# Optimization experiments

Hardware: AMD Instinct MI355X
Metric: run time of the kernel (lower is better)

Reference implementation:

```python
import jax, jax.numpy as jnp
import numpy as np

B, M = 4, 4096          # events x points-per-event (row_splits are uniform)
N = B * M
IN_DIM, SPACE, PROP, K = 128, 4, 64, 32


def setup_inputs() -> dict:
    key = jax.random.key(0)
    k1, k2, k3, k4, k5 = jax.random.split(key, 5)
    x = jax.random.normal(k1, (N, IN_DIM), jnp.float32)
    row_splits = (jnp.arange(B + 1, dtype=jnp.int32) * M)
    s = 1.0 / np.sqrt(IN_DIM)
    Ws = jax.random.uniform(k2, (IN_DIM, SPACE), jnp.float32, -s, s)
    bs = jax.random.uniform(k3, (SPACE,), jnp.float32, -s, s)
    Wp = jax.random.uniform(k4, (IN_DIM, PROP), jnp.float32, -s, s)
    bp = jax.random.uniform(k5, (PROP,), jnp.float32, -s, s)
    return {"x": x, "Ws": Ws, "bs": bs, "Wp": Wp, "bp": bp, "row_splits": row_splits}


def _gravnet(x, Ws, bs, Wp, bp):
    space = x @ Ws + bs                      # [N, SPACE] learned coordinates
    prop = x @ Wp + bp                       # [N, PROP]  features to propagate
    sp = space.reshape(B, M, SPACE)
    pr = prop.reshape(B, M, PROP)
    # exact KNN within each event (row_splits segment): pairwise squared dists
    sq = jnp.sum(sp * sp, axis=-1)                         # [B, M]
    d2 = sq[:, :, None] + sq[:, None, :] - 2.0 * jnp.einsum("bms,bns->bmn", sp, sp)
    neg_vals, idx = jax.lax.top_k(-d2, K)                  # k smallest dists (incl. self)
    distsq = jnp.maximum(-neg_vals, 0.0)                   # [B, M, K]
    weights = jnp.exp(-10.0 * distsq)                      # [B, M, K]
    gathered = jax.vmap(lambda p, i: p[i])(pr, idx)        # [B, M, K, PROP]
    weighted = gathered * weights[..., None]
    fmean = jnp.mean(weighted, axis=2)                     # [B, M, PROP]
    fmax = jnp.max(weighted, axis=2)                       # [B, M, PROP]
    out = jnp.concatenate([fmean, fmax], axis=-1)          # [B, M, 2*PROP]
    return out.reshape(N, 2 * PROP)


def reference(x, Ws, bs, Wp, bp, row_splits):
    # row_splits encodes uniform segments [0, M, 2M, ...]; KNN never crosses them.
    return _gravnet(x, Ws, bs, Wp, bp)
```

## Files before the change

### kernel.cpp

```cpp
#include <hip/hip_runtime.h>
#include <hip/hip_bf16.h>
#include <math.h>

#define N_TOT   16384
#define M_EV    4096
#define IN_DIM  128
#define SPACE_D 4
#define PROP_D  64
#define K_NN    32
#define CAND_CAP 128
#define MARGIN  0.04f

typedef _Float16 h2 __attribute__((ext_vector_type(2)));
typedef unsigned long long u64;

__device__ __forceinline__ h2 pkmin(h2 a, h2 b) {
#if __has_builtin(__builtin_elementwise_min)
  return __builtin_elementwise_min(a, b);
#else
  h2 r; r.x = (a.x < b.x) ? a.x : b.x; r.y = (a.y < b.y) ? a.y : b.y; return r;
#endif
}

__device__ __forceinline__ h2 pkrtz(float a, float b) {
  return __builtin_bit_cast(h2, __builtin_amdgcn_cvt_pkrtz(a, b));
}

__global__ __launch_bounds__(256) void linear_kernel(
    const float* __restrict__ x,
    const float* __restrict__ Ws, const float* __restrict__ bs,
    const float* __restrict__ Wp, const float* __restrict__ bp,
    float* __restrict__ space, float* __restrict__ prop)
{
  const int lane = threadIdx.x & 63;
  const int wid  = threadIdx.x >> 6;
  const int r0   = __builtin_amdgcn_readfirstlane((int)blockIdx.x * 16 + wid * 4);

  const float* xr = x + (size_t)r0 * IN_DIM;

  float a0 = bp[lane];
  float a1 = a0, a2 = a0, a3 = a0;
  #pragma unroll
  for (int i = 0; i < IN_DIM; ++i) {
    const float w = Wp[i * PROP_D + lane];
    a0 = fmaf(xr[i],              w, a0);
    a1 = fmaf(xr[IN_DIM + i],     w, a1);
    a2 = fmaf(xr[2 * IN_DIM + i], w, a2);
    a3 = fmaf(xr[3 * IN_DIM + i], w, a3);
  }
  prop[(size_t)(r0 + 0) * PROP_D + lane] = a0;
  prop[(size_t)(r0 + 1) * PROP_D + lane] = a1;
  prop[(size_t)(r0 + 2) * PROP_D + lane] = a2;
  prop[(size_t)(r0 + 3) * PROP_D + lane] = a3;

  if (lane < 16) {
    const int r = lane >> 2, c = lane & 3;
    const float* xq = x + (size_t)(r0 + r) * IN_DIM;
    float a = bs[c];
    #pragma unroll
    for (int i = 0; i < IN_DIM; ++i)
      a = fmaf(xq[i], Ws[i * SPACE_D + c], a);
    space[(size_t)(r0 + r) * SPACE_D + c] = a;
  }
}

__device__ __forceinline__ int mbcnt64(u64 mk) {
  return (int)__builtin_amdgcn_mbcnt_hi((unsigned)(mk >> 32),
           __builtin_amdgcn_mbcnt_lo((unsigned)mk, 0u));
}

__global__ __launch_bounds__(512, 8) void knn_kernel(
    const float4* __restrict__ space,
    const float*  __restrict__ prop,
    float*        __restrict__ out)
{
  const int lane = threadIdx.x & 63;
  const int wid  = threadIdx.x >> 6;
  const int row  = (int)blockIdx.x * 8 + wid;
  const int m0   = row & ~(M_EV - 1);
  const int mloc = row & (M_EV - 1);

  __shared__ uint4 s_pk[M_EV / 2];
  __shared__ int   s_ci[8][CAND_CAP];
  __shared__ uint2 s_w[8][K_NN];
  __shared__ int   s_cnt[8];

  {
    const float4* src = space + m0;
    #pragma unroll
    for (int it = 0; it < 4; ++it) {
      const int i = (int)threadIdx.x + it * 512;
      const float4 a = src[i];
      const float4 b = src[i + 2048];
      s_pk[i] = make_uint4(
        __builtin_bit_cast(unsigned, pkrtz(a.x, b.x)),
        __builtin_bit_cast(unsigned, pkrtz(a.y, b.y)),
        __builtin_bit_cast(unsigned, pkrtz(a.z, b.z)),
        __builtin_bit_cast(unsigned, pkrtz(a.w, b.w)));
    }
  }
  if (lane == 0) s_cnt[wid] = 0;
  __syncthreads();

  const float4 qf = space[m0 + mloc];
  const h2 qx = pkrtz(qf.x, qf.x), qy = pkrtz(qf.y, qf.y);
  const h2 qz = pkrtz(qf.z, qf.z), qw = pkrtz(qf.w, qf.w);

  unsigned pd[32];
  h2 mn; mn.x = (_Float16)65504.f; mn.y = (_Float16)65504.f;
  #pragma unroll
  for (int t = 0; t < 32; ++t) {
    const uint4 u = s_pk[lane + (t << 6)];
    const h2 dx = qx - __builtin_bit_cast(h2, u.x);
    const h2 dy = qy - __builtin_bit_cast(h2, u.y);
    const h2 dz = qz - __builtin_bit_cast(h2, u.z);
    const h2 dw = qw - __builtin_bit_cast(h2, u.w);
    h2 s = dx * dx;
    s = dy * dy + s;
    s = dz * dz + s;
    s = dw * dw + s;
    pd[t] = __builtin_bit_cast(unsigned, s);
    mn = pkmin(mn, s);
  }

  const unsigned mnbits = __builtin_bit_cast(unsigned, mn);
  const unsigned c0 = mnbits & 0xFFFFu, c1 = mnbits >> 16;
  unsigned blo = 0u, bhi = 0x7C00u;
  while (blo < bhi) {
    const unsigned mid = (blo + bhi) >> 1;
    const int c = (int)__popcll(__ballot(c0 <= mid)) +
                  (int)__popcll(__ballot(c1 <= mid));
    if (c >= K_NN) { bhi = mid; if (c == K_NN) break; }
    else blo = mid + 1;
  }
  const float T = (float)__builtin_bit_cast(_Float16, (unsigned short)bhi) + MARGIN;
  const h2 Th = pkrtz(T, T);

  #pragma unroll
  for (int t = 0; t < 32; ++t) asm volatile("" : "+v"(pd[t]));

  #pragma unroll
  for (int t = 0; t < 32; ++t) {
    const h2 s = __builtin_bit_cast(h2, pd[t]);
    if (s.x <= Th.x) {
      const int pos = atomicAdd(&s_cnt[wid], 1);
      if (pos < CAND_CAP) s_ci[wid][pos] = (t << 6) + lane;
    }
    if (s.y <= Th.y) {
      const int pos = atomicAdd(&s_cnt[wid], 1);
      if (pos < CAND_CAP) s_ci[wid][pos] = (t << 6) + lane + 2048;
    }
  }
  int C = s_cnt[wid];

  if (C > CAND_CAP) {
    const float4* __restrict__ ev = space + m0;
    unsigned lo = 0u, hi = __float_as_uint(T);
    while (lo < hi) {
      const unsigned mid = (lo + hi) >> 1;
      const float fm = __uint_as_float(mid);
      int c = 0;
      #pragma unroll 1
      for (int t = 0; t < 64; ++t) {
        const float4 cc = ev[lane + (t << 6)];
        const float dx = qf.x - cc.x, dy = qf.y - cc.y;
        const float dz = qf.z - cc.z, dw = qf.w - cc.w;
        const float dd = fmaf(dx, dx, fmaf(dy, dy, fmaf(dz, dz, dw * dw)));
        c += (int)__popcll(__ballot(dd <= fm));
      }
      if (c >= K_NN) { hi = mid; if (c == K_NN) break; }
      else lo = mid + 1;
    }
    const float Tf = __uint_as_float(hi);
    int cnt = 0;
    #pragma unroll 1
    for (int pass = 0; pass < 2; ++pass) {
      #pragma unroll 1
      for (int t = 0; t < 64; ++t) {
        const float4 cc = ev[lane + (t << 6)];
        const float dx = qf.x - cc.x, dy = qf.y - cc.y;
        const float dz = qf.z - cc.z, dw = qf.w - cc.w;
        const float dd = fmaf(dx, dx, fmaf(dy, dy, fmaf(dz, dz, dw * dw)));
        const bool p = pass ? (dd == Tf) : (dd < Tf);
        const u64 mk = __ballot(p);
        if (p) {
          const int pos = cnt + mbcnt64(mk);
          if (pos < K_NN) s_ci[wid][pos] = (t << 6) + lane;
        }
        cnt += (int)__popcll(mk);
      }
      if (cnt >= K_NN) break;
    }
    C = K_NN;
  }

  const bool h0 = (lane < C), h1 = (64 + lane < C);
  const int i0 = h0 ? s_ci[wid][lane]      : 0;
  const int i1 = h1 ? s_ci[wid][64 + lane] : 0;
  float v0 = INFINITY, v1 = INFINITY;
  if (h0) {
    const float4 cc = space[m0 + i0];
    const float dx = qf.x - cc.x, dy = qf.y - cc.y;
    const float dz = qf.z - cc.z, dw = qf.w - cc.w;
    v0 = fmaf(dx, dx, fmaf(dy, dy, fmaf(dz, dz, dw * dw)));
  }
  if (h1) {
    const float4 cc = space[m0 + i1];
    const float dx = qf.x - cc.x, dy = qf.y - cc.y;
    const float dz = qf.z - cc.z, dw = qf.w - cc.w;
    v1 = fmaf(dx, dx, fmaf(dy, dy, fmaf(dz, dz, dw * dw)));
  }

  unsigned lo = 0u, hi = __float_as_uint(T);
  while (lo < hi) {
    const unsigned mid = (lo + hi) >> 1;
    const float fm = __uint_as_float(mid);
    const int c = (int)__popcll(__ballot(v0 <= fm)) +
                  (int)__popcll(__ballot(v1 <= fm));
    if (c >= K_NN) { hi = mid; if (c == K_NN) break; }
    else lo = mid + 1;
  }
  const float T2 = __uint_as_float(hi);

  const u64 mkE0 = __ballot(v0 == T2);
  const u64 mkE1 = __ballot(v1 == T2);
  const int L = (int)__popcll(__ballot(v0 < T2)) +
                (int)__popcll(__ballot(v1 < T2));
  const int e = K_NN - L;
  const int nE0 = (int)__popcll(mkE0);
  const bool sel0 = (v0 < T2) || ((v0 == T2) && (mbcnt64(mkE0) < e));
  const bool sel1 = (v1 < T2) || ((v1 == T2) && (nE0 + mbcnt64(mkE1) < e));

  const float w0 = __expf(-10.f * v0);
  const float w1 = __expf(-10.f * v1);

  {
    const u64 mkS0 = __ballot(sel0);
    if (sel0) {
      const int pos = mbcnt64(mkS0);
      s_w[wid][pos] = make_uint2((unsigned)i0, __float_as_uint(w0));
    }
    const int b0 = (int)__popcll(mkS0);
    const u64 mkS1 = __ballot(sel1);
    if (sel1) {
      const int pos = b0 + mbcnt64(mkS1);
      s_w[wid][pos] = make_uint2((unsigned)i1, __float_as_uint(w1));
    }
  }

  float accm = 0.f;
  float accx = -INFINITY;
  const float* __restrict__ pb = prop + ((size_t)m0 << 6) + lane;
  #pragma unroll 8
  for (int n = 0; n < K_NN; ++n) {
    const uint2 wn = s_w[wid][n];
    const float w = __uint_as_float(wn.y);
    const float v = pb[(size_t)wn.x << 6];
    const float wv = w * v;
    accm += wv;
    accx = fmaxf(accx, wv);
  }
  out[(size_t)row * 128 + lane]      = accm * (1.f / K_NN);
  out[(size_t)row * 128 + 64 + lane] = accx;
}

extern "C" void kernel_launch(void* const* d_in, const int* in_sizes, int n_in,
                              void* d_out, int out_size, void* d_ws, size_t ws_size,
                              hipStream_t stream) {
  const float* x  = (const float*)d_in[0];
  const float* Ws = (const float*)d_in[1];
  const float* bs = (const float*)d_in[2];
  const float* Wp = (const float*)d_in[3];
  const float* bp = (const float*)d_in[4];
  float* out = (float*)d_out;

  float* prop  = (float*)d_ws;
  float* space = (float*)((char*)d_ws + (size_t)N_TOT * PROP_D * sizeof(float));

  linear_kernel<<<N_TOT / 16, 256, 0, stream>>>(x, Ws, bs, Wp, bp, space, prop);
  knn_kernel<<<N_TOT / 8, 512, 0, stream>>>((const float4*)space, prop, out);
}
```

Measured before the change: 52.99 us.

## Compute KNN distance prefilter with MFMA and process 32 query rows per block

Replaces the per-query packed-fp16 distance scan with MFMA 16x16x32 fp16 matrix products computing -2q·c plus a precomputed |c|^2 term. Each block now handles 32 queries: per-lane partial minima are reduced into a threshold per row, and a second MFMA pass collects candidates with atomic appends. The exact fp32 refinement, selection and gather stages are kept, run per row by each wave. The aim is to cut the VALU cost of the all-pairs scan and amortize the shared-memory staging of the event over more queries, at the cost of doing the MFMA pass twice, lower occupancy, and a fp16 expanded-form approximation that relies on a larger margin.

```diff
diff --git a/kernel.cpp b/kernel.cpp
--- a/kernel.cpp
+++ b/kernel.cpp
@@ -9,21 +9,27 @@
 #define PROP_D  64
 #define K_NN    32
 #define CAND_CAP 128
-#define MARGIN  0.04f
+#define M_SCALED 0.25f
 
 typedef _Float16 h2 __attribute__((ext_vector_type(2)));
+typedef __attribute__((ext_vector_type(8))) _Float16 h16x8;
+typedef __attribute__((ext_vector_type(4))) float f32x4;
 typedef unsigned long long u64;
-
-__device__ __forceinline__ h2 pkmin(h2 a, h2 b) {
-#if __has_builtin(__builtin_elementwise_min)
-  return __builtin_elementwise_min(a, b);
-#else
-  h2 r; r.x = (a.x < b.x) ? a.x : b.x; r.y = (a.y < b.y) ? a.y : b.y; return r;
-#endif
-}
 
 __device__ __forceinline__ h2 pkrtz(float a, float b) {
   return __builtin_bit_cast(h2, __builtin_amdgcn_cvt_pkrtz(a, b));
+}
+__device__ __forceinline__ unsigned fmap(float f) {
+  unsigned b = __float_as_uint(f);
+  return (b & 0x80000000u) ? ~b : (b | 0x80000000u);
+}
+__device__ __forceinline__ float funmap(unsigned u) {
+  unsigned b = (u & 0x80000000u) ? (u & 0x7FFFFFFFu) : ~u;
+  return __uint_as_float(b);
+}
+__device__ __forceinline__ int mbcnt64(u64 mk) {
+  return (int)__builtin_amdgcn_mbcnt_hi((unsigned)(mk >> 32),
+           __builtin_amdgcn_mbcnt_lo((unsigned)mk, 0u));
 }
 
 __global__ __launch_bounds__(256) void linear_kernel(
@@ -64,204 +70,242 @@
   }
 }
 
-__device__ __forceinline__ int mbcnt64(u64 mk) {
-  return (int)__builtin_amdgcn_mbcnt_hi((unsigned)(mk >> 32),
-           __builtin_amdgcn_mbcnt_lo((unsigned)mk, 0u));
-}
-
-__global__ __launch_bounds__(512, 8) void knn_kernel(
+__global__ __launch_bounds__(512, 4) void knn_kernel(
     const float4* __restrict__ space,
     const float*  __restrict__ prop,
     float*        __restrict__ out)
 {
   const int lane = threadIdx.x & 63;
   const int wid  = threadIdx.x >> 6;
-  const int row  = (int)blockIdx.x * 8 + wid;
-  const int m0   = row & ~(M_EV - 1);
-  const int mloc = row & (M_EV - 1);
-
-  __shared__ uint4 s_pk[M_EV / 2];
-  __shared__ int   s_ci[8][CAND_CAP];
-  __shared__ uint2 s_w[8][K_NN];
-  __shared__ int   s_cnt[8];
+  const int rt   = wid >> 2;
+  const int qq   = wid & 3;
+  const int brow0 = (int)blockIdx.x * 32;
+  const int m0    = brow0 & ~(M_EV - 1);
+  const int ml0   = brow0 & (M_EV - 1);
+
+  __shared__ uint2          s_B[M_EV];
+  __shared__ float          s_c2[M_EV];
+  __shared__ float          s_pmin[32][64];
+  __shared__ float          s_T[32];
+  __shared__ unsigned short s_ci[32][CAND_CAP];
+  __shared__ int            s_cnt[32];
+  __shared__ uint2          s_w[32][K_NN];
 
   {
     const float4* src = space + m0;
     #pragma unroll
-    for (int it = 0; it < 4; ++it) {
+    for (int it = 0; it < 8; ++it) {
       const int i = (int)threadIdx.x + it * 512;
-      const float4 a = src[i];
-      const float4 b = src[i + 2048];
-      s_pk[i] = make_uint4(
-        __builtin_bit_cast(unsigned, pkrtz(a.x, b.x)),
-        __builtin_bit_cast(unsigned, pkrtz(a.y, b.y)),
-        __builtin_bit_cast(unsigned, pkrtz(a.z, b.z)),
-        __builtin_bit_cast(unsigned, pkrtz(a.w, b.w)));
-    }
-  }
-  if (lane == 0) s_cnt[wid] = 0;
+      const float4 c = src[i];
+      s_B[i] = make_uint2(
+          __builtin_bit_cast(unsigned, pkrtz(c.x, c.y)),
+          __builtin_bit_cast(unsigned, pkrtz(c.z, c.w)));
+      s_c2[i] = 8.f * fmaf(c.x, c.x, fmaf(c.y, c.y, fmaf(c.z, c.z, c.w * c.w)));
+    }
+  }
+  if (threadIdx.x < 32) s_cnt[threadIdx.x] = 0;
   __syncthreads();
 
-  const float4 qf = space[m0 + mloc];
-  const h2 qx = pkrtz(qf.x, qf.x), qy = pkrtz(qf.y, qf.y);
-  const h2 qz = pkrtz(qf.z, qf.z), qw = pkrtz(qf.w, qf.w);
-
-  unsigned pd[32];
-  h2 mn; mn.x = (_Float16)65504.f; mn.y = (_Float16)65504.f;
+  const float4 qa = space[m0 + ml0 + rt * 16 + (lane & 15)];
+  const unsigned a01 = __builtin_bit_cast(unsigned, pkrtz(-2.f * qa.x, -2.f * qa.y));
+  const unsigned a23 = __builtin_bit_cast(unsigned, pkrtz(-2.f * qa.z, -2.f * qa.w));
+  uint4 au; au.x = a01; au.y = a23; au.z = a01; au.w = a23;
+  const h16x8 afrag = __builtin_bit_cast(h16x8, au);
+
+  const int cbase = qq * 1024;
+
+  f32x4 mna = {INFINITY, INFINITY, INFINITY, INFINITY};
+  #pragma unroll 8
+  for (int t = 0; t < 64; ++t) {
+    const int cb = cbase + t * 16;
+    const uint2 b = s_B[cb + (lane & 15)];
+    const float c2s = s_c2[cb + (lane & 15)];
+    uint4 bu; bu.x = b.x; bu.y = b.y; bu.z = b.x; bu.w = b.y;
+    const h16x8 bfrag = __builtin_bit_cast(h16x8, bu);
+    f32x4 acc = {0.f, 0.f, 0.f, 0.f};
+    acc = __builtin_amdgcn_mfma_f32_16x16x32_f16(afrag, bfrag, acc, 0, 0, 0);
+    #pragma unroll
+    for (int j = 0; j < 4; ++j) {
+      const float v = acc[j] + c2s;
+      mna[j] = fminf(mna[j], v);
+    }
+  }
+  {
+    const int r16 = (lane >> 4) * 4;
+    #pragma unroll
+    for (int j = 0; j < 4; ++j)
+      s_pmin[rt * 16 + r16 + j][qq * 16 + (lane & 15)] = mna[j];
+  }
+  __syncthreads();
+
   #pragma unroll
-  for (int t = 0; t < 32; ++t) {
-    const uint4 u = s_pk[lane + (t << 6)];
-    const h2 dx = qx - __builtin_bit_cast(h2, u.x);
-    const h2 dy = qy - __builtin_bit_cast(h2, u.y);
-    const h2 dz = qz - __builtin_bit_cast(h2, u.z);
-    const h2 dw = qw - __builtin_bit_cast(h2, u.w);
-    h2 s = dx * dx;
-    s = dy * dy + s;
-    s = dz * dz + s;
-    s = dw * dw + s;
-    pd[t] = __builtin_bit_cast(unsigned, s);
-    mn = pkmin(mn, s);
-  }
-
-  const unsigned mnbits = __builtin_bit_cast(unsigned, mn);
-  const unsigned c0 = mnbits & 0xFFFFu, c1 = mnbits >> 16;
-  unsigned blo = 0u, bhi = 0x7C00u;
-  while (blo < bhi) {
-    const unsigned mid = (blo + bhi) >> 1;
-    const int c = (int)__popcll(__ballot(c0 <= mid)) +
-                  (int)__popcll(__ballot(c1 <= mid));
-    if (c >= K_NN) { bhi = mid; if (c == K_NN) break; }
-    else blo = mid + 1;
-  }
-  const float T = (float)__builtin_bit_cast(_Float16, (unsigned short)bhi) + MARGIN;
-  const h2 Th = pkrtz(T, T);
-
-  #pragma unroll
-  for (int t = 0; t < 32; ++t) asm volatile("" : "+v"(pd[t]));
-
-  #pragma unroll
-  for (int t = 0; t < 32; ++t) {
-    const h2 s = __builtin_bit_cast(h2, pd[t]);
-    if (s.x <= Th.x) {
-      const int pos = atomicAdd(&s_cnt[wid], 1);
-      if (pos < CAND_CAP) s_ci[wid][pos] = (t << 6) + lane;
-    }
-    if (s.y <= Th.y) {
-      const int pos = atomicAdd(&s_cnt[wid], 1);
-      if (pos < CAND_CAP) s_ci[wid][pos] = (t << 6) + lane + 2048;
-    }
-  }
-  int C = s_cnt[wid];
-
-  if (C > CAND_CAP) {
-    const float4* __restrict__ ev = space + m0;
-    unsigned lo = 0u, hi = __float_as_uint(T);
+  for (int rr = 0; rr < 4; ++rr) {
+    const int br = wid * 4 + rr;
+    const unsigned u = fmap(s_pmin[br][lane]);
+    unsigned lo = 0u, hi = 0xFFFFFFFFu;
     while (lo < hi) {
-      const unsigned mid = (lo + hi) >> 1;
-      const float fm = __uint_as_float(mid);
-      int c = 0;
-      #pragma unroll 1
-      for (int t = 0; t < 64; ++t) {
-        const float4 cc = ev[lane + (t << 6)];
-        const float dx = qf.x - cc.x, dy = qf.y - cc.y;
-        const float dz = qf.z - cc.z, dw = qf.w - cc.w;
-        const float dd = fmaf(dx, dx, fmaf(dy, dy, fmaf(dz, dz, dw * dw)));
-        c += (int)__popcll(__ballot(dd <= fm));
-      }
+      const unsigned mid = lo + ((hi - lo) >> 1);
+      const int c = (int)__popcll(__ballot(u <= mid));
       if (c >= K_NN) { hi = mid; if (c == K_NN) break; }
       else lo = mid + 1;
     }
-    const float Tf = __uint_as_float(hi);
-    int cnt = 0;
-    #pragma unroll 1
-    for (int pass = 0; pass < 2; ++pass) {
+    if (lane == 0) s_T[br] = funmap(hi) + M_SCALED;
+  }
+  __syncthreads();
+
+  {
+    const int r16 = (lane >> 4) * 4;
+    int   rowj[4];
+    float Tj[4];
+    #pragma unroll
+    for (int j = 0; j < 4; ++j) {
+      rowj[j] = rt * 16 + r16 + j;
+      Tj[j]   = s_T[rowj[j]];
+    }
+    #pragma unroll 8
+    for (int t = 0; t < 64; ++t) {
+      const int cb = cbase + t * 16;
+      const uint2 b = s_B[cb + (lane & 15)];
+      const float c2s = s_c2[cb + (lane & 15)];
+      uint4 bu; bu.x = b.x; bu.y = b.y; bu.z = b.x; bu.w = b.y;
+      const h16x8 bfrag = __builtin_bit_cast(h16x8, bu);
+      f32x4 acc = {0.f, 0.f, 0.f, 0.f};
+      acc = __builtin_amdgcn_mfma_f32_16x16x32_f16(afrag, bfrag, acc, 0, 0, 0);
+      #pragma unroll
+      for (int j = 0; j < 4; ++j) {
+        const float v = acc[j] + c2s;
+        if (v <= Tj[j]) {
+          const int pos = atomicAdd(&s_cnt[rowj[j]], 1);
+          s_ci[rowj[j]][pos & (CAND_CAP - 1)] =
+              (unsigned short)(cb + (lane & 15));
+        }
+      }
+    }
+  }
+  __syncthreads();
+
+  const float* __restrict__ pb = prop + ((size_t)m0 << 6) + lane;
+  #pragma unroll 1
+  for (int rr = 0; rr < 4; ++rr) {
+    const int br   = wid * 4 + rr;
+    const int rloc = ml0 + br;
+    const int grow = brow0 + br;
+    int C = s_cnt[br];
+
+    const float4 qf = space[m0 + rloc];
+    const float q2f = fmaf(qf.x, qf.x, fmaf(qf.y, qf.y,
+                      fmaf(qf.z, qf.z, qf.w * qf.w)));
+    float Tt = s_T[br] * 0.125f + q2f;
+    if (Tt < 0.f) Tt = 0.f;
+
+    if (C > CAND_CAP) {
+      const float4* __restrict__ ev = space + m0;
+      unsigned lo = 0u, hi = __float_as_uint(Tt);
+      while (lo < hi) {
+        const unsigned mid = lo + ((hi - lo) >> 1);
+        const float fm = __uint_as_float(mid);
+        int c = 0;
+        #pragma unroll 1
+        for (int t = 0; t < 64; ++t) {
+          const float4 cc = ev[lane + (t << 6)];
+          const float dx = qf.x - cc.x, dy = qf.y - cc.y;
+          const float dz = qf.z - cc.z, dw = qf.w - cc.w;
+          const float dd = fmaf(dx, dx, fmaf(dy, dy, fmaf(dz, dz, dw * dw)));
+          c += (int)__popcll(__ballot(dd <= fm));
+        }
+        if (c >= K_NN) { hi = mid; if (c == K_NN) break; }
+        else lo = mid + 1;
+      }
+      const float Tf = __uint_as_float(hi);
+      int cnt = 0;
       #pragma unroll 1
-      for (int t = 0; t < 64; ++t) {
-        const float4 cc = ev[lane + (t << 6)];
-        const float dx = qf.x - cc.x, dy = qf.y - cc.y;
-        const float dz = qf.z - cc.z, dw = qf.w - cc.w;
-        const float dd = fmaf(dx, dx, fmaf(dy, dy, fmaf(dz, dz, dw * dw)));
-        const bool p = pass ? (dd == Tf) : (dd < Tf);
-        const u64 mk = __ballot(p);
-        if (p) {
-          const int pos = cnt + mbcnt64(mk);
-          if (pos < K_NN) s_ci[wid][pos] = (t << 6) + lane;
+      for (int pass = 0; pass < 2; ++pass) {
+        #pragma unroll 1
+        for (int t = 0; t < 64; ++t) {
+          const float4 cc = ev[lane + (t << 6)];
+          const float dx = qf.x - cc.x, dy = qf.y - cc.y;
+          const float dz = qf.z - cc.z, dw = qf.w - cc.w;
+          const float dd = fmaf(dx, dx, fmaf(dy, dy, fmaf(dz, dz, dw * dw)));
+          const bool p = pass ? (dd == Tf) : (dd < Tf);
+          const u64 mk = __ballot(p);
+          if (p) {
+            const int pos = cnt + mbcnt64(mk);
+            if (pos < K_NN) s_ci[br][pos] = (unsigned short)((t << 6) + lane);
+          }
+          cnt += (int)__popcll(mk);
         }
-        cnt += (int)__popcll(mk);
-      }
-      if (cnt >= K_NN) break;
-    }
-    C = K_NN;
-  }
-
-  const bool h0 = (lane < C), h1 = (64 + lane < C);
-  const int i0 = h0 ? s_ci[wid][lane]      : 0;
-  const int i1 = h1 ? s_ci[wid][64 + lane] : 0;
-  float v0 = INFINITY, v1 = INFINITY;
-  if (h0) {
-    const float4 cc = space[m0 + i0];
-    const float dx = qf.x - cc.x, dy = qf.y - cc.y;
-    const float dz = qf.z - cc.z, dw = qf.w - cc.w;
-    v0 = fmaf(dx, dx, fmaf(dy, dy, fmaf(dz, dz, dw * dw)));
-  }
-  if (h1) {
-    const float4 cc = space[m0 + i1];
-    const float dx = qf.x - cc.x, dy = qf.y - cc.y;
-    const float dz = qf.z - cc.z, dw = qf.w - cc.w;
-    v1 = fmaf(dx, dx, fmaf(dy, dy, fmaf(dz, dz, dw * dw)));
-  }
-
-  unsigned lo = 0u, hi = __float_as_uint(T);
-  while (lo < hi) {
-    const unsigned mid = (lo + hi) >> 1;
-    const float fm = __uint_as_float(mid);
-    const int c = (int)__popcll(__ballot(v0 <= fm)) +
-                  (int)__popcll(__ballot(v1 <= fm));
-    if (c >= K_NN) { hi = mid; if (c == K_NN) break; }
-    else lo = mid + 1;
-  }
-  const float T2 = __uint_as_float(hi);
-
-  const u64 mkE0 = __ballot(v0 == T2);
-  const u64 mkE1 = __ballot(v1 == T2);
-  const int L = (int)__popcll(__ballot(v0 < T2)) +
-                (int)__popcll(__ballot(v1 < T2));
-  const int e = K_NN - L;
-  const int nE0 = (int)__popcll(mkE0);
-  const bool sel0 = (v0 < T2) || ((v0 == T2) && (mbcnt64(mkE0) < e));
-  const bool sel1 = (v1 < T2) || ((v1 == T2) && (nE0 + mbcnt64(mkE1) < e));
-
-  const float w0 = __expf(-10.f * v0);
-  const float w1 = __expf(-10.f * v1);
-
-  {
-    const u64 mkS0 = __ballot(sel0);
-    if (sel0) {
-      const int pos = mbcnt64(mkS0);
-      s_w[wid][pos] = make_uint2((unsigned)i0, __float_as_uint(w0));
-    }
-    const int b0 = (int)__popcll(mkS0);
-    const u64 mkS1 = __ballot(sel1);
-    if (sel1) {
-      const int pos = b0 + mbcnt64(mkS1);
-      s_w[wid][pos] = make_uint2((unsigned)i1, __float_as_uint(w1));
-    }
-  }
-
-  float accm = 0.f;
-  float accx = -INFINITY;
-  const float* __restrict__ pb = prop + ((size_t)m0 << 6) + lane;
-  #pragma unroll 8
-  for (int n = 0; n < K_NN; ++n) {
-    const uint2 wn = s_w[wid][n];
-    const float w = __uint_as_float(wn.y);
-    const float v = pb[(size_t)wn.x << 6];
-    const float wv = w * v;
-    accm += wv;
-    accx = fmaxf(accx, wv);
-  }
-  out[(size_t)row * 128 + lane]      = accm * (1.f / K_NN);
-  out[(size_t)row * 128 + 64 + lane] = accx;
+        if (cnt >= K_NN) break;
+      }
+      C = K_NN;
+    }
+
+    const bool h0 = (lane < C), h1 = (64 + lane < C);
+    const int i0 = h0 ? (int)s_ci[br][lane]      : 0;
+    const int i1 = h1 ? (int)s_ci[br][64 + lane] : 0;
+    float v0 = INFINITY, v1 = INFINITY;
+    if (h0) {
+      const float4 cc = space[m0 + i0];
+      const float dx = qf.x - cc.x, dy = qf.y - cc.y;
+      const float dz = qf.z - cc.z, dw = qf.w - cc.w;
+      v0 = fmaf(dx, dx, fmaf(dy, dy, fmaf(dz, dz, dw * dw)));
+    }
+    if (h1) {
+      const float4 cc = space[m0 + i1];
+      const float dx = qf.x - cc.x, dy = qf.y - cc.y;
+      const float dz = qf.z - cc.z, dw = qf.w - cc.w;
+      v1 = fmaf(dx, dx, fmaf(dy, dy, fmaf(dz, dz, dw * dw)));
+    }
+
+    unsigned lo = 0u, hi = __float_as_uint(Tt);
+    while (lo < hi) {
+      const unsigned mid = lo + ((hi - lo) >> 1);
+      const float fm = __uint_as_float(mid);
+      const int c = (int)__popcll(__ballot(v0 <= fm)) +
+                    (int)__popcll(__ballot(v1 <= fm));
+      if (c >= K_NN) { hi = mid; if (c == K_NN) break; }
+      else lo = mid + 1;
+    }
+    const float T2 = __uint_as_float(hi);
+
+    const u64 mkE0 = __ballot(v0 == T2);
+    const u64 mkE1 = __ballot(v1 == T2);
+    const int L = (int)__popcll(__ballot(v0 < T2)) +
+                  (int)__popcll(__ballot(v1 < T2));
+    const int e = K_NN - L;
+    const int nE0 = (int)__popcll(mkE0);
+    const bool sel0 = (v0 < T2) || ((v0 == T2) && (mbcnt64(mkE0) < e));
+    const bool sel1 = (v1 < T2) || ((v1 == T2) && (nE0 + mbcnt64(mkE1) < e));
+
+    const float w0 = __expf(-10.f * v0);
+    const float w1 = __expf(-10.f * v1);
+    {
+      const u64 mkS0 = __ballot(sel0);
+      if (sel0) {
+        const int pos = mbcnt64(mkS0);
+        s_w[br][pos] = make_uint2((unsigned)i0, __float_as_uint(w0));
+      }
+      const int b0 = (int)__popcll(mkS0);
+      const u64 mkS1 = __ballot(sel1);
+      if (sel1) {
+        const int pos = b0 + mbcnt64(mkS1);
+        s_w[br][pos] = make_uint2((unsigned)i1, __float_as_uint(w1));
+      }
+    }
+
+    float accm = 0.f;
+    float accx = -INFINITY;
+    #pragma unroll 8
+    for (int n = 0; n < K_NN; ++n) {
+      const uint2 wn = s_w[br][n];
+      const float w = __uint_as_float(wn.y);
+      const float v = pb[(size_t)wn.x << 6];
+      const float wv = w * v;
+      accm += wv;
+      accx = fmaxf(accx, wv);
+    }
+    out[(size_t)grow * 128 + lane]      = accm * (1.f / K_NN);
+    out[(size_t)grow * 128 + 64 + lane] = accx;
+  }
 }
 
 extern "C" void kernel_launch(void* const* d_in, const int* in_sizes, int n_in,
@@ -278,5 +322,5 @@
   float* space = (float*)((char*)d_ws + (size_t)N_TOT * PROP_D * sizeof(float));
 
   linear_kernel<<<N_TOT / 16, 256, 0, stream>>>(x, Ws, bs, Wp, bp, space, prop);
-  knn_kernel<<<N_TOT / 8, 512, 0, stream>>>((const float4*)space, prop, out);
-}
+  knn_kernel<<<N_TOT / 32, 512, 0, stream>>>((const float4*)space, prop, out);
+}
```

Measured after the change: 69.85 us. 31.8% more time.
